# Kernel optimization log

Hardware: AMD Instinct MI355X
Metric: run time of the kernel (lower is better)

## Reference

```python
import jax, jax.numpy as jnp
import numpy as np

THRES = 0.5
EPS = 1e-8
FACTOR = 5


def _row_normalize(mx):
    # torch: rowsum over last dim, 1/rowsum with inf->0, diag @ mx == row scaling
    r_inv = 1.0 / mx.sum(-1)
    r_inv = jnp.where(jnp.isinf(r_inv), 0.0, r_inv)
    return mx * r_inv[..., None]


def _build_adj(feat):
    # cosine-similarity adjacency over rows of feat [B,N,D] -> [B,N,N]
    fn = feat / jnp.maximum(jnp.linalg.norm(feat, axis=-1, keepdims=True), EPS)
    sim = jnp.einsum('bnd,bmd->bnm', fn, fn)
    adj = (sim > THRES).astype(feat.dtype)
    adjT = jnp.swapaxes(adj, 1, 2)
    m = (adjT > adj).astype(feat.dtype)
    adj = adj + adjT * m - adj * m  # symmetric OR
    return _row_normalize(adj + jnp.eye(adj.shape[1], dtype=feat.dtype))


def _gcn(x, adj, w1, b1, w2, b2):
    # standard 2-layer pygcn: out = adj @ (x @ W) + b, relu between, dropout=0
    h = jax.nn.relu(jnp.einsum('bnm,bmf->bnf', adj, x @ w1) + b1)
    return jnp.einsum('bnm,bmf->bnf', adj, h @ w2) + b2


def setup_inputs() -> dict:
    key = jax.random.key(0)
    ks = jax.random.split(key, 13)
    B, C, HT = 1024, 64, 128   # batch, in_dim channels, height == feature_len
    FL, NH = 128, 8            # GCN nfeat/nclass, nhid
    s = lambda i, shape: jax.random.normal(ks[i], shape, jnp.float32) * 0.1
    return dict(
        x=jax.random.normal(ks[0], (B, C, HT), jnp.float32),
        wq=s(1, (C, C)), bq=s(2, (C,)),
        wk=s(3, (C, C)), bk=s(4, (C,)),
        wv=s(5, (C, C)), bv=s(6, (C,)),
        gw1=s(7, (FL, NH)), gb1=s(8, (NH,)),
        gw2=s(9, (NH, FL)), gb2=s(10, (FL,)),
        gamma=jax.random.normal(ks[11], (), jnp.float32),
        index_sample=jax.random.randint(ks[12], (HT, 25), 0, HT),  # (L_Q_inner, sample_k)
    )


def reference(x, wq, bq, wk, bk, wv, bv, gw1, gb1, gw2, gb2, gamma, index_sample):
    # 1x1 Conv1d projections: [B,C,H] -> [B,C,H]
    q = jnp.einsum('oc,bch->boh', wq, x) + bq[None, :, None]
    k = jnp.einsum('oc,bch->boh', wk, x) + bk[None, :, None]
    v = jnp.einsum('oc,bch->boh', wv, x) + bv[None, :, None]

    def branch(f):
        # source uses self.gcn_query for all three branches (faithful)
        return _gcn(_row_normalize(f), _build_adj(f), gw1, gb1, gw2, gb2)

    queries, keys, values = branch(q), branch(k), branch(v)
    B, L_Q, H = queries.shape        # [B, 64, 128]
    u = min(FACTOR * int(np.ceil(np.log(L_Q))), L_Q)  # n_top = 25

    # ProbSparse _prob_QK: inner view (B, Hn=64, Lk=128)
    Lk = keys.shape[2]
    Kg = keys[:, :, index_sample]                        # [B,64,Lk,S] gather
    qk_sample = jnp.einsum('bhl,bhls->bhs', queries, Kg)  # [B,64,S]
    M = qk_sample.max(-1) - qk_sample.sum(-1) / Lk        # [B,64]
    _, m_top = jax.lax.top_k(M, u)                        # [B,u] indices over node dim
    q_red = jnp.take_along_axis(queries, m_top[:, :, None], axis=1)  # [B,u,128]
    scores = jnp.einsum('bud,bnd->bun', q_red, keys) * (1.0 / np.sqrt(H))

    # mask_flag=True -> initial context is cumsum over nodes
    context = jnp.cumsum(values, axis=-2)                 # [B,64,128]
    attn = jax.nn.softmax(scores, axis=-1)
    upd = jnp.einsum('bun,bnd->bud', attn, values)        # [B,u,128]
    context = context.at[jnp.arange(B)[:, None], m_top].set(upd)
    return gamma * context + x
```

## Files before the change

kernel.cpp:

```cpp
#include <hip/hip_runtime.h>
#include <math.h>

#define T 1024
#define FS 132
#define FSQ 33
#define AS 68
#define ASQ 17

typedef __attribute__((ext_vector_type(8)))  short short8;
typedef __attribute__((ext_vector_type(4)))  float f32x4;
typedef __attribute__((ext_vector_type(16))) float f32x16;

__device__ __forceinline__ void macc(float& acc, const float4 a, const float4 b) {
  acc = fmaf(a.x, b.x, acc);
  acc = fmaf(a.y, b.y, acc);
  acc = fmaf(a.z, b.z, acc);
  acc = fmaf(a.w, b.w, acc);
}
__device__ __forceinline__ void fma4(float4& a, float s, const float4 b) {
  a.x = fmaf(s, b.x, a.x);
  a.y = fmaf(s, b.y, a.y);
  a.z = fmaf(s, b.z, a.z);
  a.w = fmaf(s, b.w, a.w);
}
__device__ __forceinline__ unsigned bf16rne(float f) {
  unsigned u = __float_as_uint(f);
  return (u + 0x7FFFu + ((u >> 16) & 1u)) >> 16;
}
__device__ __forceinline__ void split3(float4 a, float4 b, short8& vh, short8& vm, short8& vl) {
  const float xs[8] = {a.x, a.y, a.z, a.w, b.x, b.y, b.z, b.w};
#pragma unroll
  for (int e = 0; e < 8; ++e) {
    float x = xs[e];
    unsigned h = bf16rne(x);
    float r1 = x - __uint_as_float(h << 16);
    unsigned m = bf16rne(r1);
    float r2 = r1 - __uint_as_float(m << 16);
    unsigned l2 = bf16rne(r2);
    vh[e] = (short)h; vm[e] = (short)m; vl[e] = (short)l2;
  }
}
__device__ __forceinline__ void split2(float4 a, float4 b, short8& vh, short8& vl) {
  const float xs[8] = {a.x, a.y, a.z, a.w, b.x, b.y, b.z, b.w};
#pragma unroll
  for (int e = 0; e < 8; ++e) {
    float x = xs[e];
    unsigned h = bf16rne(x);
    float r1 = x - __uint_as_float(h << 16);
    unsigned l2 = bf16rne(r1);
    vh[e] = (short)h; vl[e] = (short)l2;
  }
}
__device__ __forceinline__ f32x16 mm32(short8 a, short8 b, f32x16 c) {
  return __builtin_amdgcn_mfma_f32_32x32x16_bf16(a, b, c, 0, 0, 0);
}
__device__ __forceinline__ f32x4 mm16(short8 a, short8 b, f32x4 c) {
  return __builtin_amdgcn_mfma_f32_16x16x32_bf16(a, b, c, 0, 0, 0);
}

__global__ __launch_bounds__(T) void gcn_ssa_kernel(
    const float* __restrict__ x,
    const float* __restrict__ wq, const float* __restrict__ bq,
    const float* __restrict__ wk, const float* __restrict__ bk,
    const float* __restrict__ wv, const float* __restrict__ bv,
    const float* __restrict__ gw1, const float* __restrict__ gb1,
    const float* __restrict__ gw2, const float* __restrict__ gb2,
    const float* __restrict__ gammap, const int* __restrict__ idxg,
    float* __restrict__ out)
{
  const int b = blockIdx.x, tid = threadIdx.x;
  const int l = tid & 63;
  const float* xb = x + (size_t)b * 8192;
  float* outb = out + (size_t)b * 8192;

  __shared__ __align__(16) float fq[64 * FS];
  __shared__ __align__(16) float fk[64 * FS];
  __shared__ __align__(16) float fv[64 * FS];
  __shared__ __align__(16) float U[12480];
  __shared__ __align__(16) float gw1T[8 * FS];
  __shared__ __align__(16) float gw2s[8 * 128];
  __shared__ __align__(16) float gb1s[8];
  __shared__ __align__(16) float gb2s[128];
  __shared__ float rinv_s[64], nrm_s[64], rinv2_s[64];
  __shared__ int mte[32];

  float4* fq4 = (float4*)fq;
  float4* fk4 = (float4*)fk;
  float4* fv4 = (float4*)fv;
  float4* U4 = (float4*)U;

  {
    const float4* xg = (const float4*)xb;
    for (int i = tid; i < 2048; i += T) {
      int r = i >> 5, cq = i & 31;
      fv4[r * FSQ + cq] = xg[i];
    }
    const float4* wqg = (const float4*)wq;
    const float4* wkg = (const float4*)wk;
    const float4* wvg = (const float4*)wv;
    for (int i = tid; i < 1024; i += T) {
      U4[i] = wqg[i];
      U4[1024 + i] = wkg[i];
      U4[2048 + i] = wvg[i];
    }
    if (tid < 64) {
      U[12288 + tid] = bq[tid];
      U[12352 + tid] = bk[tid];
      U[12416 + tid] = bv[tid];
    }
    for (int i = tid; i < 1024; i += T) {
      int h = i >> 3, j = i & 7;
      gw1T[j * FS + h] = gw1[i];
      gw2s[i] = gw2[i];
    }
    if (tid < 8) gb1s[tid] = gb1[tid];
    if (tid < 128) gb2s[tid] = gb2[tid];
  }
  __syncthreads();

  float4 vacc0, vacc1;
  {
    const int o0 = (tid >> 5) << 1;
    const int hq = tid & 31;
    const float4* wqs = U4;
    const float4* wks = U4 + 1024;
    const float4* wvs = U4 + 2048;
    float4 aq0, aq1, ak0, ak1, av0, av1;
    {
      float bq0 = U[12288 + o0], bq1 = U[12288 + o0 + 1];
      float bk0 = U[12352 + o0], bk1 = U[12352 + o0 + 1];
      float bv0 = U[12416 + o0], bv1 = U[12416 + o0 + 1];
      aq0 = make_float4(bq0, bq0, bq0, bq0); aq1 = make_float4(bq1, bq1, bq1, bq1);
      ak0 = make_float4(bk0, bk0, bk0, bk0); ak1 = make_float4(bk1, bk1, bk1, bk1);
      av0 = make_float4(bv0, bv0, bv0, bv0); av1 = make_float4(bv1, bv1, bv1, bv1);
    }
    for (int cq = 0; cq < 16; ++cq) {
      float4 x0 = fv4[(4 * cq + 0) * FSQ + hq];
      float4 x1 = fv4[(4 * cq + 1) * FSQ + hq];
      float4 x2 = fv4[(4 * cq + 2) * FSQ + hq];
      float4 x3 = fv4[(4 * cq + 3) * FSQ + hq];
      float4 w;
      w = wqs[o0 * 16 + cq];       fma4(aq0, w.x, x0); fma4(aq0, w.y, x1); fma4(aq0, w.z, x2); fma4(aq0, w.w, x3);
      w = wqs[(o0 + 1) * 16 + cq]; fma4(aq1, w.x, x0); fma4(aq1, w.y, x1); fma4(aq1, w.z, x2); fma4(aq1, w.w, x3);
      w = wks[o0 * 16 + cq];       fma4(ak0, w.x, x0); fma4(ak0, w.y, x1); fma4(ak0, w.z, x2); fma4(ak0, w.w, x3);
      w = wks[(o0 + 1) * 16 + cq]; fma4(ak1, w.x, x0); fma4(ak1, w.y, x1); fma4(ak1, w.z, x2); fma4(ak1, w.w, x3);
      w = wvs[o0 * 16 + cq];       fma4(av0, w.x, x0); fma4(av0, w.y, x1); fma4(av0, w.z, x2); fma4(av0, w.w, x3);
      w = wvs[(o0 + 1) * 16 + cq]; fma4(av1, w.x, x0); fma4(av1, w.y, x1); fma4(av1, w.z, x2); fma4(av1, w.w, x3);
    }
    fq4[o0 * FSQ + hq] = aq0;
    fq4[(o0 + 1) * FSQ + hq] = aq1;
    fk4[o0 * FSQ + hq] = ak0;
    fk4[(o0 + 1) * FSQ + hq] = ak1;
    vacc0 = av0; vacc1 = av1;
  }
  __syncthreads();
  {
    const int o0 = (tid >> 5) << 1, hq = tid & 31;
    fv4[o0 * FSQ + hq] = vacc0;
    fv4[(o0 + 1) * FSQ + hq] = vacc1;
  }
  __syncthreads();

  float* adjb = U;
  float* t1T = U + 4352;
  float* hT  = U + 4896;
  float* gsm = U + 5440;
  float4* adj4 = (float4*)adjb;

  for (int brr = 0; brr < 3; ++brr) {
    float* f = (brr == 0) ? fq : (brr == 1) ? fk : fv;
    float4* f4 = (float4*)f;

    {
      int row = tid >> 4, g = tid & 15;
      float4 aa = f4[row * FSQ + 2 * g];
      float4 c = f4[row * FSQ + 2 * g + 1];
      float s0 = aa.x + aa.y + aa.z + aa.w + c.x + c.y + c.z + c.w;
      float s1 = aa.x * aa.x + aa.y * aa.y + aa.z * aa.z + aa.w * aa.w +
                 c.x * c.x + c.y * c.y + c.z * c.z + c.w * c.w;
      for (int off = 8; off; off >>= 1) {
        s0 += __shfl_xor(s0, off);
        s1 += __shfl_xor(s1, off);
      }
      if (g == 0) {
        rinv_s[row] = (s0 == 0.0f) ? 0.0f : (1.0f / s0);
        nrm_s[row] = 1.0f / fmaxf(sqrtf(s1), 1e-8f);
      }
    }
    __syncthreads();

    if (tid < 256) {
      const int w = tid >> 6;
      const int r0 = (w >> 1) * 32, c0 = (w & 1) * 32;
      const int lr = l & 31;
      const int kg = (l >> 5) * 4;
      f32x16 acc = (f32x16)0.f;
      for (int ks = 0; ks < 8; ++ks) {
        int kb = ks * 16;
        float4 a0 = *(const float4*)(f + (r0 + lr) * FS + kb + kg);
        float4 a1 = *(const float4*)(f + (r0 + lr) * FS + kb + 8 + kg);
        float4 b0 = *(const float4*)(f + (c0 + lr) * FS + kb + kg);
        float4 b1 = *(const float4*)(f + (c0 + lr) * FS + kb + 8 + kg);
        short8 ah, am, al2, bh, bm, bl;
        split3(a0, a1, ah, am, al2);
        split3(b0, b1, bh, bm, bl);
        acc = mm32(ah, bh, acc);
        acc = mm32(ah, bm, acc);
        acc = mm32(am, bh, acc);
        acc = mm32(ah, bl, acc);
        acc = mm32(al2, bh, acc);
        acc = mm32(am, bm, acc);
      }
      float nm = nrm_s[c0 + lr];
#pragma unroll
      for (int reg = 0; reg < 16; ++reg) {
        int r = r0 + (reg & 3) + 8 * (reg >> 2) + 4 * (l >> 5);
        int m = c0 + lr;
        float sim = acc[reg] * nrm_s[r] * nm;
        float aa = (sim > 0.5f) ? 1.0f : 0.0f;
        if (r == m) aa += 1.0f;
        adjb[r * AS + m] = aa;
      }
    } else if (tid >= 512 && tid < 768) {
      int lt = tid - 512;
      int n = lt >> 2, j0 = (lt & 3) * 2;
      float a0 = 0.f, a1 = 0.f;
      const float4* w0 = (const float4*)(gw1T + j0 * FS);
      const float4* w1 = (const float4*)(gw1T + (j0 + 1) * FS);
      for (int hc = 0; hc < 32; ++hc) {
        float4 fx = f4[n * FSQ + hc];
        macc(a0, fx, w0[hc]);
        macc(a1, fx, w1[hc]);
      }
      float rv = rinv_s[n];
      t1T[j0 * AS + n] = a0 * rv;
      t1T[(j0 + 1) * AS + n] = a1 * rv;
    }
    __syncthreads();

    {
      int row = tid >> 4, g = tid & 15;
      float4 aa = adj4[row * ASQ + g];
      float s = aa.x + aa.y + aa.z + aa.w;
      for (int off = 8; off; off >>= 1) s += __shfl_xor(s, off);
      if (g == 0) rinv2_s[row] = 1.0f / s;
    }
    __syncthreads();

    if (tid < 512) {
      int n = tid >> 3, j = tid & 7;
      float acc = 0.f;
      const float4* a4 = (const float4*)(adjb + n * AS);
      const float4* t4 = (const float4*)(t1T + j * AS);
      for (int mq = 0; mq < 16; ++mq) macc(acc, a4[mq], t4[mq]);
      hT[j * AS + n] = fmaxf(acc * rinv2_s[n] + gb1s[j], 0.0f);
    }
    __syncthreads();

    if (tid < 512) {
      int n = tid >> 3, j = tid & 7;
      float acc = 0.f;
      const float4* a4 = (const float4*)(adjb + n * AS);
      const float4* h4 = (const float4*)(hT + j * AS);
      for (int mq = 0; mq < 16; ++mq) macc(acc, a4[mq], h4[mq]);
      gsm[n * 8 + j] = acc * rinv2_s[n];
    }
    __syncthreads();

    {
      int n0 = tid >> 5, hq = tid & 31;
      int n1 = n0 + 32;
      const float4* g4 = (const float4*)gsm;
      float4 ga0 = g4[n0 * 2], ga1 = g4[n0 * 2 + 1];
      float4 gc0 = g4[n1 * 2], gc1 = g4[n1 * 2 + 1];
      const float* pa0 = (const float*)&ga0;
      const float* pa1 = (const float*)&ga1;
      const float* pc0 = (const float*)&gc0;
      const float* pc1 = (const float*)&gc1;
      const float4* w4 = (const float4*)gw2s;
      float4 bquad = ((const float4*)gb2s)[hq];
      float4 acc0 = bquad, acc1 = bquad;
#pragma unroll
      for (int j = 0; j < 4; ++j) {
        float4 w = w4[j * 32 + hq];
        fma4(acc0, pa0[j], w);
        fma4(acc1, pc0[j], w);
      }
#pragma unroll
      for (int j = 0; j < 4; ++j) {
        float4 w = w4[(j + 4) * 32 + hq];
        fma4(acc0, pa1[j], w);
        fma4(acc1, pc1[j], w);
      }
      f4[n0 * FSQ + hq] = acc0;
      f4[n1 * FSQ + hq] = acc1;
    }
    __syncthreads();
  }

  float* kT = U;
  float* Pp = U + 8704;
  {
    const int c = tid >> 6;
    const int n = tid & 63;
    float4 v0 = fk4[n * FSQ + 2 * c];
    float4 v1 = fk4[n * FSQ + 2 * c + 1];
    const float* p0 = (const float*)&v0;
    const float* p1 = (const float*)&v1;
#pragma unroll
    for (int e = 0; e < 4; ++e) kT[(8 * c + e) * AS + n] = p0[e];
#pragma unroll
    for (int e = 0; e < 4; ++e) kT[(8 * c + 4 + e) * AS + n] = p1[e];
  }
  __syncthreads();

  const float gamma = *gammap;
  if (tid < 128) {
    const int w = tid >> 6, n = l;
    float acc[25];
#pragma unroll
    for (int s = 0; s < 25; ++s) acc[s] = 0.f;
    const float* qrow = fq + n * FS + w * 64;
    for (int lb = 0; lb < 16; ++lb) {
      float4 qv = *(const float4*)(qrow + 4 * lb);
      const float* qp = (const float*)&qv;
#pragma unroll
      for (int i = 0; i < 4; ++i) {
        const float qs = qp[i];
        const int base = __builtin_amdgcn_readfirstlane((w * 64 + 4 * lb + i) * 25);
#pragma unroll
        for (int s = 0; s < 25; ++s) {
          acc[s] = fmaf(qs, kT[idxg[base + s] * AS + n], acc[s]);
        }
      }
    }
    float* P = Pp + w * 1600;
#pragma unroll
    for (int s = 0; s < 25; ++s) P[s * 64 + n] = acc[s];
  } else if (tid < 256) {
    const int h = tid - 128;
    float acc = 0.f;
    for (int n = 0; n < 64; ++n) {
      acc += fv[n * FS + h];
      outb[n * 128 + h] = fmaf(gamma, acc, xb[n * 128 + h]);
    }
  }
  __syncthreads();

  if (tid < 64) {
    if (tid >= 25 && tid < 32) mte[tid] = 0;
    const float* P0 = Pp;
    const float* P1 = Pp + 1600;
    float mx = -INFINITY, su = 0.f;
#pragma unroll
    for (int s = 0; s < 25; ++s) {
      float vsum = P0[s * 64 + tid] + P1[s * 64 + tid];
      mx = fmaxf(mx, vsum);
      su += vsum;
    }
    float v = mx - su * (1.0f / 128.0f);
    for (int it = 0; it < 25; ++it) {
      float bv2 = v;
      int bi = tid;
#pragma unroll
      for (int off = 32; off > 0; off >>= 1) {
        float ov = __shfl_xor(bv2, off);
        int oi = __shfl_xor(bi, off);
        if (ov > bv2 || (ov == bv2 && oi < bi)) { bv2 = ov; bi = oi; }
      }
      if (tid == 0) mte[it] = bi;
      if (tid == bi) v = -INFINITY;
    }
  }
  __syncthreads();

  float* sc = U + 8704;
  float* vT = U;
  if (tid < 128) {
    const int w = tid >> 6;
    const int lr = l & 31;
    const int kg = (l >> 5) * 4;
    const int qr = mte[lr];
    const float scale = 0.08838834764831845f;
    f32x16 acc = (f32x16)0.f;
    for (int ks = 0; ks < 8; ++ks) {
      int kb = ks * 16;
      float4 a0 = *(const float4*)(fq + qr * FS + kb + kg);
      float4 a1 = *(const float4*)(fq + qr * FS + kb + 8 + kg);
      float4 b0 = *(const float4*)(fk + (w * 32 + lr) * FS + kb + kg);
      float4 b1 = *(const float4*)(fk + (w * 32 + lr) * FS + kb + 8 + kg);
      short8 ah, al2, bh, bl;
      split2(a0, a1, ah, al2);
      split2(b0, b1, bh, bl);
      acc = mm32(ah, bh, acc);
      acc = mm32(ah, bl, acc);
      acc = mm32(al2, bh, acc);
    }
#pragma unroll
    for (int reg = 0; reg < 16; ++reg) {
      int uu = (reg & 3) + 8 * (reg >> 2) + 4 * (l >> 5);
      if (uu < 25) sc[uu * AS + w * 32 + lr] = acc[reg] * scale;
    }
  } else {
    for (int i = tid - 128; i < 8192; i += 896) {
      int h2 = i >> 6, n = i & 63;
      vT[h2 * AS + n] = fv[n * FS + h2];
    }
  }
  __syncthreads();

  if (tid < 400) {
    int u = tid >> 4, g = tid & 15;
    float4* s4 = (float4*)(sc + u * AS);
    float4 v = s4[g];
    float mx = fmaxf(fmaxf(v.x, v.y), fmaxf(v.z, v.w));
    for (int off = 8; off; off >>= 1) mx = fmaxf(mx, __shfl_xor(mx, off));
    float4 e;
    e.x = __expf(v.x - mx); e.y = __expf(v.y - mx);
    e.z = __expf(v.z - mx); e.w = __expf(v.w - mx);
    float su = e.x + e.y + e.z + e.w;
    for (int off = 8; off; off >>= 1) su += __shfl_xor(su, off);
    float inv = 1.0f / su;
    e.x *= inv; e.y *= inv; e.z *= inv; e.w *= inv;
    s4[g] = e;
  }
  __syncthreads();

  if (tid < 512) {
    const int w = tid >> 6;
    const int li = l & 15;
    const int kg4 = (l >> 4) * 4;
#pragma unroll
    for (int i = 0; i < 2; ++i) {
      int t = w * 2 + i;
      int ut = t >> 3, ht = t & 7;
      int u = ut * 16 + li;
      f32x4 acc = (f32x4)0.f;
#pragma unroll
      for (int ks = 0; ks < 2; ++ks) {
        int kb = ks * 32;
        float4 a0 = *(const float4*)(sc + u * AS + kb + kg4);
        float4 a1 = *(const float4*)(sc + u * AS + kb + 16 + kg4);
        float4 b0 = *(const float4*)(vT + (ht * 16 + li) * AS + kb + kg4);
        float4 b1 = *(const float4*)(vT + (ht * 16 + li) * AS + kb + 16 + kg4);
        short8 ah, al2, bh, bl;
        split2(a0, a1, ah, al2);
        split2(b0, b1, bh, bl);
        acc = mm16(ah, bh, acc);
        acc = mm16(ah, bl, acc);
        acc = mm16(al2, bh, acc);
      }
      int hcol = ht * 16 + li;
#pragma unroll
      for (int r = 0; r < 4; ++r) {
        int uu = ut * 16 + (l >> 4) * 4 + r;
        if (uu < 25) {
          int row = mte[uu];
          int o = row * 128 + hcol;
          outb[o] = fmaf(gamma, acc[r], xb[o]);
        }
      }
    }
  }
}

extern "C" void kernel_launch(void* const* d_in, const int* in_sizes, int n_in,
                              void* d_out, int out_size, void* d_ws, size_t ws_size,
                              hipStream_t stream) {
  const float* x   = (const float*)d_in[0];
  const float* wq  = (const float*)d_in[1];
  const float* bq  = (const float*)d_in[2];
  const float* wk  = (const float*)d_in[3];
  const float* bk  = (const float*)d_in[4];
  const float* wv  = (const float*)d_in[5];
  const float* bv  = (const float*)d_in[6];
  const float* gw1 = (const float*)d_in[7];
  const float* gb1 = (const float*)d_in[8];
  const float* gw2 = (const float*)d_in[9];
  const float* gb2 = (const float*)d_in[10];
  const float* gm  = (const float*)d_in[11];
  const int* idx   = (const int*)d_in[12];
  float* out = (float*)d_out;
  int B = in_sizes[0] / (64 * 128);
  hipLaunchKernelGGL(gcn_ssa_kernel, dim3(B), dim3(T), 0, stream,
                     x, wq, bq, wk, bk, wv, bv, gw1, gb1, gw2, gb2, gm, idx, out);
}
```

Baseline: 303.3 us.

## Batch three GCN branches concurrently and move projections and GCN matmuls to MFMA

Replaces the scalar FMA 1x1-conv projection with split-bf16 MFMA tiles reading a transposed copy of x. The three GCN branches now run together instead of in a sequential loop, which cuts the number of barrier-separated phases. The adjacency is stored as bf16 so that adj@t1 and adj@h run on 16x16 MFMA, and x@W1 uses MFMA with a zero-padded weight. The risk is extra split-bf16 rounding work and a larger shared-memory footprint.

After: 296.6 us. -2.2%, faster.

```diff
diff --git a/kernel.cpp b/kernel.cpp
--- a/kernel.cpp
+++ b/kernel.cpp
@@ -5,18 +5,13 @@
 #define FS 132
 #define FSQ 33
 #define AS 68
-#define ASQ 17
 
 typedef __attribute__((ext_vector_type(8)))  short short8;
 typedef __attribute__((ext_vector_type(4)))  float f32x4;
 typedef __attribute__((ext_vector_type(16))) float f32x16;
-
-__device__ __forceinline__ void macc(float& acc, const float4 a, const float4 b) {
-  acc = fmaf(a.x, b.x, acc);
-  acc = fmaf(a.y, b.y, acc);
-  acc = fmaf(a.z, b.z, acc);
-  acc = fmaf(a.w, b.w, acc);
-}
+typedef __attribute__((ext_vector_type(4)))  unsigned u32x4;
+typedef __attribute__((ext_vector_type(2)))  unsigned u32x2;
+
 __device__ __forceinline__ void fma4(float4& a, float s, const float4 b) {
   a.x = fmaf(s, b.x, a.x);
   a.y = fmaf(s, b.y, a.y);
@@ -70,233 +65,270 @@
 {
   const int b = blockIdx.x, tid = threadIdx.x;
   const int l = tid & 63;
+  const int wid = tid >> 6;
   const float* xb = x + (size_t)b * 8192;
   float* outb = out + (size_t)b * 8192;
 
   __shared__ __align__(16) float fq[64 * FS];
   __shared__ __align__(16) float fk[64 * FS];
   __shared__ __align__(16) float fv[64 * FS];
-  __shared__ __align__(16) float U[12480];
-  __shared__ __align__(16) float gw1T[8 * FS];
-  __shared__ __align__(16) float gw2s[8 * 128];
+  __shared__ __align__(16) float U[11904];
+  __shared__ __align__(16) float gw1T[16 * FS];
   __shared__ __align__(16) float gb1s[8];
   __shared__ __align__(16) float gb2s[128];
-  __shared__ float rinv_s[64], nrm_s[64], rinv2_s[64];
+  __shared__ float rinv_s[3][64], nrm_s[3][64], rinv2_s[3][64];
   __shared__ int mte[32];
 
   float4* fq4 = (float4*)fq;
   float4* fk4 = (float4*)fk;
   float4* fv4 = (float4*)fv;
-  float4* U4 = (float4*)U;
 
   {
     const float4* xg = (const float4*)xb;
     for (int i = tid; i < 2048; i += T) {
-      int r = i >> 5, cq = i & 31;
-      fv4[r * FSQ + cq] = xg[i];
-    }
-    const float4* wqg = (const float4*)wq;
-    const float4* wkg = (const float4*)wk;
-    const float4* wvg = (const float4*)wv;
-    for (int i = tid; i < 1024; i += T) {
-      U4[i] = wqg[i];
-      U4[1024 + i] = wkg[i];
-      U4[2048 + i] = wvg[i];
-    }
-    if (tid < 64) {
-      U[12288 + tid] = bq[tid];
-      U[12352 + tid] = bk[tid];
-      U[12416 + tid] = bv[tid];
-    }
-    for (int i = tid; i < 1024; i += T) {
-      int h = i >> 3, j = i & 7;
-      gw1T[j * FS + h] = gw1[i];
-      gw2s[i] = gw2[i];
+      int c = i & 63, hq = i >> 6;
+      float4 v = xg[c * 32 + hq];
+      int h = hq * 4;
+      U[(h + 0) * AS + c] = v.x;
+      U[(h + 1) * AS + c] = v.y;
+      U[(h + 2) * AS + c] = v.z;
+      U[(h + 3) * AS + c] = v.w;
+    }
+    if (tid < 192) U[8704 + tid] = (tid < 64) ? bq[tid] : (tid < 128) ? bk[tid - 64] : bv[tid - 128];
+    for (int i = tid; i < 2048; i += T) {
+      int j = i >> 7, h = i & 127;
+      gw1T[j * FS + h] = (j < 8) ? gw1[h * 8 + j] : 0.f;
     }
     if (tid < 8) gb1s[tid] = gb1[tid];
     if (tid < 128) gb2s[tid] = gb2[tid];
   }
   __syncthreads();
 
-  float4 vacc0, vacc1;
+  if (wid < 12) {
+    const int p = wid >> 2, strip = wid & 3;
+    const float* wsel = (p == 0) ? wq : (p == 1) ? wk : wv;
+    float* fdst = (p == 0) ? fq : (p == 1) ? fk : fv;
+    const int lr = l & 31, kg = (l >> 5) * 4;
+    const int h = strip * 32 + lr;
+    f32x16 acc0 = (f32x16)0.f, acc1 = (f32x16)0.f;
+    for (int ks = 0; ks < 4; ++ks) {
+      int kb = ks * 16;
+      float4 b0 = *(const float4*)(U + h * AS + kb + kg);
+      float4 b1 = *(const float4*)(U + h * AS + kb + 8 + kg);
+      short8 bh, bm, bl;
+      split3(b0, b1, bh, bm, bl);
+      float4 a0 = *(const float4*)(wsel + lr * 64 + kb + kg);
+      float4 a1 = *(const float4*)(wsel + lr * 64 + kb + 8 + kg);
+      short8 ah, am, al;
+      split3(a0, a1, ah, am, al);
+      acc0 = mm32(ah, bh, acc0); acc0 = mm32(ah, bm, acc0); acc0 = mm32(am, bh, acc0);
+      acc0 = mm32(ah, bl, acc0); acc0 = mm32(al, bh, acc0); acc0 = mm32(am, bm, acc0);
+      a0 = *(const float4*)(wsel + (32 + lr) * 64 + kb + kg);
+      a1 = *(const float4*)(wsel + (32 + lr) * 64 + kb + 8 + kg);
+      split3(a0, a1, ah, am, al);
+      acc1 = mm32(ah, bh, acc1); acc1 = mm32(ah, bm, acc1); acc1 = mm32(am, bh, acc1);
+      acc1 = mm32(ah, bl, acc1); acc1 = mm32(al, bh, acc1); acc1 = mm32(am, bm, acc1);
+    }
+#pragma unroll
+    for (int reg = 0; reg < 16; ++reg) {
+      int ro = (reg & 3) + 8 * (reg >> 2) + 4 * (l >> 5);
+      fdst[ro * FS + h] = acc0[reg] + U[8704 + p * 64 + ro];
+      fdst[(32 + ro) * FS + h] = acc1[reg] + U[8704 + p * 64 + 32 + ro];
+    }
+  }
+  __syncthreads();
+
   {
-    const int o0 = (tid >> 5) << 1;
-    const int hq = tid & 31;
-    const float4* wqs = U4;
-    const float4* wks = U4 + 1024;
-    const float4* wvs = U4 + 2048;
-    float4 aq0, aq1, ak0, ak1, av0, av1;
-    {
-      float bq0 = U[12288 + o0], bq1 = U[12288 + o0 + 1];
-      float bk0 = U[12352 + o0], bk1 = U[12352 + o0 + 1];
-      float bv0 = U[12416 + o0], bv1 = U[12416 + o0 + 1];
-      aq0 = make_float4(bq0, bq0, bq0, bq0); aq1 = make_float4(bq1, bq1, bq1, bq1);
-      ak0 = make_float4(bk0, bk0, bk0, bk0); ak1 = make_float4(bk1, bk1, bk1, bk1);
-      av0 = make_float4(bv0, bv0, bv0, bv0); av1 = make_float4(bv1, bv1, bv1, bv1);
-    }
-    for (int cq = 0; cq < 16; ++cq) {
-      float4 x0 = fv4[(4 * cq + 0) * FSQ + hq];
-      float4 x1 = fv4[(4 * cq + 1) * FSQ + hq];
-      float4 x2 = fv4[(4 * cq + 2) * FSQ + hq];
-      float4 x3 = fv4[(4 * cq + 3) * FSQ + hq];
-      float4 w;
-      w = wqs[o0 * 16 + cq];       fma4(aq0, w.x, x0); fma4(aq0, w.y, x1); fma4(aq0, w.z, x2); fma4(aq0, w.w, x3);
-      w = wqs[(o0 + 1) * 16 + cq]; fma4(aq1, w.x, x0); fma4(aq1, w.y, x1); fma4(aq1, w.z, x2); fma4(aq1, w.w, x3);
-      w = wks[o0 * 16 + cq];       fma4(ak0, w.x, x0); fma4(ak0, w.y, x1); fma4(ak0, w.z, x2); fma4(ak0, w.w, x3);
-      w = wks[(o0 + 1) * 16 + cq]; fma4(ak1, w.x, x0); fma4(ak1, w.y, x1); fma4(ak1, w.z, x2); fma4(ak1, w.w, x3);
-      w = wvs[o0 * 16 + cq];       fma4(av0, w.x, x0); fma4(av0, w.y, x1); fma4(av0, w.z, x2); fma4(av0, w.w, x3);
-      w = wvs[(o0 + 1) * 16 + cq]; fma4(av1, w.x, x0); fma4(av1, w.y, x1); fma4(av1, w.z, x2); fma4(av1, w.w, x3);
-    }
-    fq4[o0 * FSQ + hq] = aq0;
-    fq4[(o0 + 1) * FSQ + hq] = aq1;
-    fk4[o0 * FSQ + hq] = ak0;
-    fk4[(o0 + 1) * FSQ + hq] = ak1;
-    vacc0 = av0; vacc1 = av1;
-  }
-  __syncthreads();
-  {
-    const int o0 = (tid >> 5) << 1, hq = tid & 31;
-    fv4[o0 * FSQ + hq] = vacc0;
-    fv4[(o0 + 1) * FSQ + hq] = vacc1;
-  }
-  __syncthreads();
-
-  float* adjb = U;
-  float* t1T = U + 4352;
-  float* hT  = U + 4896;
-  float* gsm = U + 5440;
-  float4* adj4 = (float4*)adjb;
-
-  for (int brr = 0; brr < 3; ++brr) {
-    float* f = (brr == 0) ? fq : (brr == 1) ? fk : fv;
-    float4* f4 = (float4*)f;
-
-    {
-      int row = tid >> 4, g = tid & 15;
-      float4 aa = f4[row * FSQ + 2 * g];
-      float4 c = f4[row * FSQ + 2 * g + 1];
-      float s0 = aa.x + aa.y + aa.z + aa.w + c.x + c.y + c.z + c.w;
+    int row = tid >> 4, g = tid & 15;
+#pragma unroll
+    for (int br = 0; br < 3; ++br) {
+      const float4* f4b = (br == 0) ? fq4 : (br == 1) ? fk4 : fv4;
+      float4 aa = f4b[row * FSQ + 2 * g];
+      float4 cc = f4b[row * FSQ + 2 * g + 1];
+      float s0 = aa.x + aa.y + aa.z + aa.w + cc.x + cc.y + cc.z + cc.w;
       float s1 = aa.x * aa.x + aa.y * aa.y + aa.z * aa.z + aa.w * aa.w +
-                 c.x * c.x + c.y * c.y + c.z * c.z + c.w * c.w;
+                 cc.x * cc.x + cc.y * cc.y + cc.z * cc.z + cc.w * cc.w;
       for (int off = 8; off; off >>= 1) {
         s0 += __shfl_xor(s0, off);
         s1 += __shfl_xor(s1, off);
       }
       if (g == 0) {
-        rinv_s[row] = (s0 == 0.0f) ? 0.0f : (1.0f / s0);
-        nrm_s[row] = 1.0f / fmaxf(sqrtf(s1), 1e-8f);
-      }
-    }
-    __syncthreads();
-
-    if (tid < 256) {
-      const int w = tid >> 6;
-      const int r0 = (w >> 1) * 32, c0 = (w & 1) * 32;
-      const int lr = l & 31;
-      const int kg = (l >> 5) * 4;
-      f32x16 acc = (f32x16)0.f;
-      for (int ks = 0; ks < 8; ++ks) {
-        int kb = ks * 16;
-        float4 a0 = *(const float4*)(f + (r0 + lr) * FS + kb + kg);
-        float4 a1 = *(const float4*)(f + (r0 + lr) * FS + kb + 8 + kg);
-        float4 b0 = *(const float4*)(f + (c0 + lr) * FS + kb + kg);
-        float4 b1 = *(const float4*)(f + (c0 + lr) * FS + kb + 8 + kg);
-        short8 ah, am, al2, bh, bm, bl;
-        split3(a0, a1, ah, am, al2);
-        split3(b0, b1, bh, bm, bl);
-        acc = mm32(ah, bh, acc);
-        acc = mm32(ah, bm, acc);
-        acc = mm32(am, bh, acc);
-        acc = mm32(ah, bl, acc);
-        acc = mm32(al2, bh, acc);
-        acc = mm32(am, bm, acc);
-      }
-      float nm = nrm_s[c0 + lr];
-#pragma unroll
-      for (int reg = 0; reg < 16; ++reg) {
-        int r = r0 + (reg & 3) + 8 * (reg >> 2) + 4 * (l >> 5);
-        int m = c0 + lr;
-        float sim = acc[reg] * nrm_s[r] * nm;
-        float aa = (sim > 0.5f) ? 1.0f : 0.0f;
-        if (r == m) aa += 1.0f;
-        adjb[r * AS + m] = aa;
-      }
-    } else if (tid >= 512 && tid < 768) {
-      int lt = tid - 512;
-      int n = lt >> 2, j0 = (lt & 3) * 2;
-      float a0 = 0.f, a1 = 0.f;
-      const float4* w0 = (const float4*)(gw1T + j0 * FS);
-      const float4* w1 = (const float4*)(gw1T + (j0 + 1) * FS);
-      for (int hc = 0; hc < 32; ++hc) {
-        float4 fx = f4[n * FSQ + hc];
-        macc(a0, fx, w0[hc]);
-        macc(a1, fx, w1[hc]);
-      }
-      float rv = rinv_s[n];
-      t1T[j0 * AS + n] = a0 * rv;
-      t1T[(j0 + 1) * AS + n] = a1 * rv;
-    }
-    __syncthreads();
-
-    {
-      int row = tid >> 4, g = tid & 15;
-      float4 aa = adj4[row * ASQ + g];
-      float s = aa.x + aa.y + aa.z + aa.w;
-      for (int off = 8; off; off >>= 1) s += __shfl_xor(s, off);
-      if (g == 0) rinv2_s[row] = 1.0f / s;
-    }
-    __syncthreads();
-
-    if (tid < 512) {
-      int n = tid >> 3, j = tid & 7;
-      float acc = 0.f;
-      const float4* a4 = (const float4*)(adjb + n * AS);
-      const float4* t4 = (const float4*)(t1T + j * AS);
-      for (int mq = 0; mq < 16; ++mq) macc(acc, a4[mq], t4[mq]);
-      hT[j * AS + n] = fmaxf(acc * rinv2_s[n] + gb1s[j], 0.0f);
-    }
-    __syncthreads();
-
-    if (tid < 512) {
-      int n = tid >> 3, j = tid & 7;
-      float acc = 0.f;
-      const float4* a4 = (const float4*)(adjb + n * AS);
-      const float4* h4 = (const float4*)(hT + j * AS);
-      for (int mq = 0; mq < 16; ++mq) macc(acc, a4[mq], h4[mq]);
-      gsm[n * 8 + j] = acc * rinv2_s[n];
-    }
-    __syncthreads();
-
-    {
-      int n0 = tid >> 5, hq = tid & 31;
-      int n1 = n0 + 32;
-      const float4* g4 = (const float4*)gsm;
-      float4 ga0 = g4[n0 * 2], ga1 = g4[n0 * 2 + 1];
-      float4 gc0 = g4[n1 * 2], gc1 = g4[n1 * 2 + 1];
-      const float* pa0 = (const float*)&ga0;
-      const float* pa1 = (const float*)&ga1;
-      const float* pc0 = (const float*)&gc0;
-      const float* pc1 = (const float*)&gc1;
-      const float4* w4 = (const float4*)gw2s;
-      float4 bquad = ((const float4*)gb2s)[hq];
-      float4 acc0 = bquad, acc1 = bquad;
-#pragma unroll
-      for (int j = 0; j < 4; ++j) {
-        float4 w = w4[j * 32 + hq];
-        fma4(acc0, pa0[j], w);
-        fma4(acc1, pc0[j], w);
-      }
-#pragma unroll
-      for (int j = 0; j < 4; ++j) {
-        float4 w = w4[(j + 4) * 32 + hq];
-        fma4(acc0, pa1[j], w);
-        fma4(acc1, pc1[j], w);
-      }
-      f4[n0 * FSQ + hq] = acc0;
-      f4[n1 * FSQ + hq] = acc1;
-    }
-    __syncthreads();
-  }
+        rinv_s[br][row] = (s0 == 0.0f) ? 0.0f : (1.0f / s0);
+        nrm_s[br][row] = 1.0f / fmaxf(sqrtf(s1), 1e-8f);
+      }
+    }
+  }
+  __syncthreads();
+
+  unsigned short* adjw = (unsigned short*)U;
+  float* t1T = U + 6912;
+  float* hT  = U + 8544;
+  float* gsm = U + 10176;
+
+  if (wid < 12) {
+    int br = wid >> 2, tile = wid & 3;
+    const float* f = (br == 0) ? fq : (br == 1) ? fk : fv;
+    int r0 = (tile >> 1) * 32, c0 = (tile & 1) * 32;
+    int lr = l & 31, kg = (l >> 5) * 4;
+    f32x16 acc = (f32x16)0.f;
+    for (int ks = 0; ks < 8; ++ks) {
+      int kb = ks * 16;
+      float4 a0 = *(const float4*)(f + (r0 + lr) * FS + kb + kg);
+      float4 a1 = *(const float4*)(f + (r0 + lr) * FS + kb + 8 + kg);
+      float4 b0 = *(const float4*)(f + (c0 + lr) * FS + kb + kg);
+      float4 b1 = *(const float4*)(f + (c0 + lr) * FS + kb + 8 + kg);
+      short8 ah, am, al, bh, bm, bl;
+      split3(a0, a1, ah, am, al);
+      split3(b0, b1, bh, bm, bl);
+      acc = mm32(ah, bh, acc); acc = mm32(ah, bm, acc); acc = mm32(am, bh, acc);
+      acc = mm32(ah, bl, acc); acc = mm32(al, bh, acc); acc = mm32(am, bm, acc);
+    }
+    float nm = nrm_s[br][c0 + lr];
+#pragma unroll
+    for (int reg = 0; reg < 16; ++reg) {
+      int rowg = r0 + (reg & 3) + 8 * (reg >> 2) + 4 * (l >> 5);
+      int m = c0 + lr;
+      float sim = acc[reg] * nrm_s[br][rowg] * nm;
+      unsigned short e = (sim > 0.5f) ? (unsigned short)0x3F80 : (unsigned short)0;
+      if (rowg == m) e = (sim > 0.5f) ? (unsigned short)0x4000 : (unsigned short)0x3F80;
+      adjw[(br * 64 + rowg) * 72 + m] = e;
+    }
+  } else {
+    int u = wid - 12;
+    int j15 = l & 15, kg4 = (l >> 4) * 4;
+    short8 gbh[4], gbm[4], gbl[4];
+#pragma unroll
+    for (int ks = 0; ks < 4; ++ks) {
+      int kb = ks * 32;
+      float4 b0 = *(const float4*)(gw1T + j15 * FS + kb + kg4);
+      float4 b1 = *(const float4*)(gw1T + j15 * FS + kb + 16 + kg4);
+      split3(b0, b1, gbh[ks], gbm[ks], gbl[ks]);
+    }
+#pragma unroll
+    for (int i = 0; i < 3; ++i) {
+      int tl = u * 3 + i;
+      int br = tl >> 2, mt = tl & 3;
+      const float* f = (br == 0) ? fq : (br == 1) ? fk : fv;
+      f32x4 acc = (f32x4)0.f;
+      for (int ks = 0; ks < 4; ++ks) {
+        int kb = ks * 32;
+        float4 a0 = *(const float4*)(f + (mt * 16 + j15) * FS + kb + kg4);
+        float4 a1 = *(const float4*)(f + (mt * 16 + j15) * FS + kb + 16 + kg4);
+        short8 ah, am, al;
+        split3(a0, a1, ah, am, al);
+        acc = mm16(ah, gbh[ks], acc); acc = mm16(ah, gbm[ks], acc); acc = mm16(am, gbh[ks], acc);
+        acc = mm16(ah, gbl[ks], acc); acc = mm16(al, gbh[ks], acc); acc = mm16(am, gbm[ks], acc);
+      }
+      if (j15 < 8) {
+#pragma unroll
+        for (int r = 0; r < 4; ++r) {
+          int n = mt * 16 + (l >> 4) * 4 + r;
+          t1T[(br * 8 + j15) * AS + n] = acc[r] * rinv_s[br][n];
+        }
+      }
+    }
+  }
+  __syncthreads();
+
+  if (tid < 768) {
+    int rid = tid >> 2, g = tid & 3;
+    int br = rid >> 6, n = rid & 63;
+    const unsigned short* rp = adjw + (br * 64 + n) * 72 + g * 16;
+    u32x4 v0 = *(const u32x4*)rp;
+    u32x4 v1 = *(const u32x4*)(rp + 8);
+    unsigned wds[8] = {v0.x, v0.y, v0.z, v0.w, v1.x, v1.y, v1.z, v1.w};
+    float s = 0.f;
+#pragma unroll
+    for (int e = 0; e < 8; ++e) {
+      s += __uint_as_float(wds[e] << 16);
+      s += __uint_as_float(wds[e] & 0xFFFF0000u);
+    }
+    s += __shfl_xor(s, 1);
+    s += __shfl_xor(s, 2);
+    if (g == 0) rinv2_s[br][n] = 1.0f / s;
+  }
+  __syncthreads();
+
+  if (tid < 768) {
+    int br = wid >> 2, mt = wid & 3;
+    int j15 = l & 15, kg4 = (l >> 4) * 4;
+    int arow = br * 64 + mt * 16 + j15;
+    f32x4 acc = (f32x4)0.f;
+#pragma unroll
+    for (int ks = 0; ks < 2; ++ks) {
+      int kb = ks * 32;
+      u32x2 lo = *(const u32x2*)(adjw + arow * 72 + kb + kg4);
+      u32x2 hi = *(const u32x2*)(adjw + arow * 72 + kb + 16 + kg4);
+      u32x4 cc; cc.x = lo.x; cc.y = lo.y; cc.z = hi.x; cc.w = hi.y;
+      short8 af = __builtin_bit_cast(short8, cc);
+      float4 b0 = *(const float4*)(t1T + (br * 8 + j15) * AS + kb + kg4);
+      float4 b1 = *(const float4*)(t1T + (br * 8 + j15) * AS + kb + 16 + kg4);
+      short8 bh, bm, bl;
+      split3(b0, b1, bh, bm, bl);
+      acc = mm16(af, bh, acc); acc = mm16(af, bm, acc); acc = mm16(af, bl, acc);
+    }
+    if (j15 < 8) {
+      float g1 = gb1s[j15];
+#pragma unroll
+      for (int r = 0; r < 4; ++r) {
+        int n = mt * 16 + (l >> 4) * 4 + r;
+        hT[(br * 8 + j15) * AS + n] = fmaxf(fmaf(acc[r], rinv2_s[br][n], g1), 0.0f);
+      }
+    }
+  }
+  __syncthreads();
+
+  if (tid < 768) {
+    int br = wid >> 2, mt = wid & 3;
+    int j15 = l & 15, kg4 = (l >> 4) * 4;
+    int arow = br * 64 + mt * 16 + j15;
+    f32x4 acc = (f32x4)0.f;
+#pragma unroll
+    for (int ks = 0; ks < 2; ++ks) {
+      int kb = ks * 32;
+      u32x2 lo = *(const u32x2*)(adjw + arow * 72 + kb + kg4);
+      u32x2 hi = *(const u32x2*)(adjw + arow * 72 + kb + 16 + kg4);
+      u32x4 cc; cc.x = lo.x; cc.y = lo.y; cc.z = hi.x; cc.w = hi.y;
+      short8 af = __builtin_bit_cast(short8, cc);
+      float4 b0 = *(const float4*)(hT + (br * 8 + j15) * AS + kb + kg4);
+      float4 b1 = *(const float4*)(hT + (br * 8 + j15) * AS + kb + 16 + kg4);
+      short8 bh, bm, bl;
+      split3(b0, b1, bh, bm, bl);
+      acc = mm16(af, bh, acc); acc = mm16(af, bm, acc); acc = mm16(af, bl, acc);
+    }
+    if (j15 < 8) {
+#pragma unroll
+      for (int r = 0; r < 4; ++r) {
+        int n = mt * 16 + (l >> 4) * 4 + r;
+        gsm[(br * 64 + n) * 8 + j15] = acc[r] * rinv2_s[br][n];
+      }
+    }
+  }
+  __syncthreads();
+
+  {
+    int n0 = tid >> 5, hq = tid & 31;
+    float4 wreg[8];
+#pragma unroll
+    for (int j = 0; j < 8; ++j) wreg[j] = ((const float4*)gw2)[j * 32 + hq];
+    float4 bquad = ((const float4*)gb2s)[hq];
+#pragma unroll
+    for (int br = 0; br < 3; ++br) {
+      float4* f4b = (br == 0) ? fq4 : (br == 1) ? fk4 : fv4;
+#pragma unroll
+      for (int half = 0; half < 2; ++half) {
+        int n = n0 + 32 * half;
+        const float* g = gsm + (br * 64 + n) * 8;
+        float4 g0 = *(const float4*)g;
+        float4 g1 = *(const float4*)(g + 4);
+        float4 a = bquad;
+        fma4(a, g0.x, wreg[0]); fma4(a, g0.y, wreg[1]); fma4(a, g0.z, wreg[2]); fma4(a, g0.w, wreg[3]);
+        fma4(a, g1.x, wreg[4]); fma4(a, g1.y, wreg[5]); fma4(a, g1.z, wreg[6]); fma4(a, g1.w, wreg[7]);
+        f4b[n * FSQ + hq] = a;
+      }
+    }
+  }
+  __syncthreads();
 
   float* kT = U;
   float* Pp = U + 8704;
@@ -377,7 +409,7 @@
   float* sc = U + 8704;
   float* vT = U;
   if (tid < 128) {
-    const int w = tid >> 6;
+    const int wsc = tid >> 6;
     const int lr = l & 31;
     const int kg = (l >> 5) * 4;
     const int qr = mte[lr];
@@ -387,8 +419,8 @@
       int kb = ks * 16;
       float4 a0 = *(const float4*)(fq + qr * FS + kb + kg);
       float4 a1 = *(const float4*)(fq + qr * FS + kb + 8 + kg);
-      float4 b0 = *(const float4*)(fk + (w * 32 + lr) * FS + kb + kg);
-      float4 b1 = *(const float4*)(fk + (w * 32 + lr) * FS + kb + 8 + kg);
+      float4 b0 = *(const float4*)(fk + (wsc * 32 + lr) * FS + kb + kg);
+      float4 b1 = *(const float4*)(fk + (wsc * 32 + lr) * FS + kb + 8 + kg);
       short8 ah, al2, bh, bl;
       split2(a0, a1, ah, al2);
       split2(b0, b1, bh, bl);
@@ -399,7 +431,7 @@
 #pragma unroll
     for (int reg = 0; reg < 16; ++reg) {
       int uu = (reg & 3) + 8 * (reg >> 2) + 4 * (l >> 5);
-      if (uu < 25) sc[uu * AS + w * 32 + lr] = acc[reg] * scale;
+      if (uu < 25) sc[uu * AS + wsc * 32 + lr] = acc[reg] * scale;
     }
   } else {
     for (int i = tid - 128; i < 8192; i += 896) {
@@ -427,12 +459,12 @@
   __syncthreads();
 
   if (tid < 512) {
-    const int w = tid >> 6;
+    const int w8 = tid >> 6;
     const int li = l & 15;
     const int kg4 = (l >> 4) * 4;
 #pragma unroll
     for (int i = 0; i < 2; ++i) {
-      int t = w * 2 + i;
+      int t = w8 * 2 + i;
       int ut = t >> 3, ht = t & 7;
       int u = ut * 16 + li;
       f32x4 acc = (f32x4)0.f;
```
